# Kernel optimization log

Measured on AMD Instinct MI355X. Metric: run time of the kernel, lower is better.

The kernel has to match this reference:

```python
import jax, jax.numpy as jnp
import numpy as np

LR = 0.1  # inner-loop learning rate from `param - 0.1 * grad`

D = 4096          # memory width d; key/val are (1, d) per docstring
CTX = 512         # loss_context_size: number of keys per update step


def setup_inputs() -> dict:
    key = jax.random.key(0)
    k1, k2, k3 = jax.random.split(key, 3)
    W = jax.random.normal(k1, (D, D), dtype=jnp.float32) / np.sqrt(D)
    keys = jax.random.normal(k2, (CTX, D), dtype=jnp.float32)
    vals = jax.random.normal(k3, (CTX, D), dtype=jnp.float32)
    return {"W": W, "keys": keys, "vals": vals}


def reference(W, keys, vals):
    # OneStep.forward: preds_i = functional_forward(key_i, (W,)) = key_i @ W,
    # loss = MSE(preds, vals); new_W = W - 0.1 * dloss/dW.
    # The per-key loop is batched into a single (CTX, D) x (D, D) matmul.
    def loss_fn(Wp):
        preds = keys @ Wp  # (CTX, D)
        return jnp.mean((preds - vals) ** 2)

    g = jax.grad(loss_fn)(W)
    return W - LR * g
```

## Files before the change

kernel.cpp:

```cpp
#include <hip/hip_runtime.h>
#include <hip/hip_bf16.h>


typedef __bf16 bf16_t;
typedef __bf16 bf16x8 __attribute__((ext_vector_type(8)));
typedef float f32x4 __attribute__((ext_vector_type(4)));

#define D_DIM 4096
#define CTX_N 512
#define UPD_SCALE 9.5367431640625e-8f

__device__ __forceinline__ void gld16(const bf16_t* g, bf16_t* l) {
    __builtin_amdgcn_global_load_lds(
        (const __attribute__((address_space(1))) void*)g,
        (__attribute__((address_space(3))) void*)l, 16, 0, 0);
}

__device__ __forceinline__ void t_body2(
    float* tile, const float* __restrict__ src, bf16_t* __restrict__ dstT,
    bf16_t* __restrict__ dstN, int M, int N, int bx, int by)
{
    const int tid = threadIdx.x;
    const int C0 = bx * 64, R0 = by * 64;
    const int r  = tid >> 2, cs = (tid & 3) * 16;

    const float* s = src + (size_t)(R0 + r) * N + C0 + cs;
    float f[16];
#pragma unroll
    for (int u = 0; u < 4; ++u) {
        const float4 v = ((const float4*)s)[u];
        f[4 * u + 0] = v.x; f[4 * u + 1] = v.y; f[4 * u + 2] = v.z; f[4 * u + 3] = v.w;
    }
#pragma unroll
    for (int u = 0; u < 16; ++u) tile[r * 65 + cs + u] = f[u];

    if (dstN) {
        bf16x8 v0, v1;
#pragma unroll
        for (int u = 0; u < 8; ++u) { v0[u] = (bf16_t)f[u]; v1[u] = (bf16_t)f[8 + u]; }
        bf16_t* d = dstN + (size_t)(R0 + r) * N + C0 + cs;
        *(bf16x8*)d = v0; *(bf16x8*)(d + 8) = v1;
    }
    __syncthreads();

    bf16x8 o0, o1;
#pragma unroll
    for (int u = 0; u < 8; ++u) {
        o0[u] = (bf16_t)tile[(cs + u) * 65 + r];
        o1[u] = (bf16_t)tile[(cs + 8 + u) * 65 + r];
    }
    bf16_t* d = dstT + (size_t)(C0 + r) * M + R0 + cs;
    *(bf16x8*)d = o0; *(bf16x8*)(d + 8) = o1;
}

__global__ __launch_bounds__(256) void t_all(
    const float* __restrict__ W, const float* __restrict__ K,
    const float* __restrict__ V, bf16_t* __restrict__ Wt,
    bf16_t* __restrict__ Kt, bf16_t* __restrict__ Kb, bf16_t* __restrict__ Vt)
{
    __shared__ float tile[64 * 65];
    const int y = blockIdx.y;
    if (y < 64)      t_body2(tile, W, Wt, nullptr, D_DIM, D_DIM, blockIdx.x, y);
    else if (y < 72) t_body2(tile, K, Kt, Kb,      CTX_N, D_DIM, blockIdx.x, y - 64);
    else             t_body2(tile, V, Vt, nullptr, CTX_N, D_DIM, blockIdx.x, y - 72);
}



#define K1_COMPUTE(BSEL, WA, WB)                                             \
    {                                                                        \
        const bf16_t* As = (const bf16_t*)(reg + (BSEL) * 8192);             \
        const bf16_t* Bs = (const bf16_t*)(reg + 4096 + (BSEL) * 8192);      \
        __builtin_amdgcn_s_waitcnt(WA);                                      \
        bf16x8 af[4];                                                        \
        _Pragma("unroll")                                                    \
        for (int mi = 0; mi < 4; ++mi)                                       \
            af[mi] = *(const bf16x8*)(As + (mi * 16 + l15) * 32 + quad * 8); \
        __builtin_amdgcn_s_waitcnt(WB);                                      \
        bf16x8 bq[4];                                                        \
        _Pragma("unroll")                                                    \
        for (int ni = 0; ni < 4; ++ni)                                       \
            bq[ni] = *(const bf16x8*)(Bs + (ni * 16 + l15) * 32 + quad * 8); \
        _Pragma("unroll")                                                    \
        for (int mi = 0; mi < 4; ++mi)                                       \
            _Pragma("unroll")                                                \
            for (int ni = 0; ni < 4; ++ni)                                   \
                acc[mi][ni] = __builtin_amdgcn_mfma_f32_16x16x32_bf16(       \
                    af[mi], bq[ni], acc[mi][ni], 0, 0, 0);                   \
    }

__global__ __launch_bounds__(256) void k1_residual(
    const bf16_t* __restrict__ Wt, const bf16_t* __restrict__ Kb,
    const bf16_t* __restrict__ Vt, bf16_t* __restrict__ Rt)
{
    __shared__ __align__(16) char smem[65536];

    const int tid = threadIdx.x, wave = tid >> 6, lane = tid & 63;
    const int j0 = blockIdx.x * 64, c0 = blockIdx.y * 64;
    const int l15 = lane & 15, quad = lane >> 4;
    const int kw = wave * 1024;

    char* reg = smem + wave * 16384;

    f32x4 acc[4][4] = {};

    const int srow = lane >> 2, sseg = (lane & 3) * 8;
    const bf16_t* ga = Wt + (size_t)(j0 + srow) * D_DIM + kw + sseg;
    const bf16_t* gb = Kb + (size_t)(c0 + srow) * D_DIM + kw + sseg;

    auto stageA = [&](int bsel, int ko) {
        bf16_t* la = (bf16_t*)(reg + bsel * 8192) + lane * 8;
#pragma unroll
        for (int c = 0; c < 4; ++c)
            gld16(ga + ko + (size_t)(c * 16) * D_DIM, la + c * 512);
    };
    auto stageB = [&](int bsel, int ko) {
        bf16_t* lb = (bf16_t*)(reg + 4096 + bsel * 8192) + lane * 8;
#pragma unroll
        for (int c = 0; c < 4; ++c)
            gld16(gb + ko + (size_t)(c * 16) * D_DIM, lb + c * 512);
    };

    stageA(0, 0); stageB(0, 0);
#pragma unroll 1
    for (int t = 1; t <= 29; t += 2) {
        stageA(1, t * 32); stageB(1, t * 32);
        __builtin_amdgcn_sched_barrier(0);
        K1_COMPUTE(0, 0x0f7c, 0x0f78);
        stageA(0, (t + 1) * 32); stageB(0, (t + 1) * 32);
        __builtin_amdgcn_sched_barrier(0);
        K1_COMPUTE(1, 0x0f7c, 0x0f78);
    }
    stageA(1, 31 * 32); stageB(1, 31 * 32);
    __builtin_amdgcn_sched_barrier(0);
    K1_COMPUTE(0, 0x0f7c, 0x0f78);
    K1_COMPUTE(1, 0x0f74, 0x0f70);

    float* ep = (float*)smem;
    __syncthreads();
#pragma unroll
    for (int w = 0; w < 4; ++w) {
        if (wave == w) {
#pragma unroll
            for (int mi = 0; mi < 4; ++mi)
#pragma unroll
                for (int ni = 0; ni < 4; ++ni)
#pragma unroll
                    for (int r = 0; r < 4; ++r) {
                        const int row = mi * 16 + quad * 4 + r;
                        const int col = ni * 16 + l15;
                        if (w == 0) ep[row * 68 + col]  = acc[mi][ni][r];
                        else        ep[row * 68 + col] += acc[mi][ni][r];
                    }
        }
        __syncthreads();
    }

    {
        const int row = tid >> 2, cs = (tid & 3) * 16;
        const size_t rbase = (size_t)(j0 + row) * CTX_N + c0 + cs;
        float e[16];
#pragma unroll
        for (int u = 0; u < 4; ++u) {
            const float4 v = ((const float4*)(ep + row * 68 + cs))[u];
            e[4 * u + 0] = v.x; e[4 * u + 1] = v.y;
            e[4 * u + 2] = v.z; e[4 * u + 3] = v.w;
        }
        const bf16x8 v0 = *(const bf16x8*)(Vt + rbase);
        const bf16x8 v1 = *(const bf16x8*)(Vt + rbase + 8);
        bf16x8 o0, o1;
#pragma unroll
        for (int u = 0; u < 8; ++u) {
            o0[u] = (bf16_t)(e[u]     - (float)v0[u]);
            o1[u] = (bf16_t)(e[8 + u] - (float)v1[u]);
        }
        *(bf16x8*)(Rt + rbase)     = o0;
        *(bf16x8*)(Rt + rbase + 8) = o1;
    }
}


#define K2_COMPUTE(BSEL)                                                     \
    {                                                                        \
        const bf16_t* As = (const bf16_t*)(smem + (BSEL) * 16384);           \
        const bf16_t* Bs = (const bf16_t*)(smem + (BSEL) * 16384 + 8192);    \
        bf16x8 af[4], bq[4];                                                 \
        _Pragma("unroll")                                                    \
        for (int mi = 0; mi < 4; ++mi)                                       \
            af[mi] = *(const bf16x8*)(As + (wi + mi * 16 + l15) * 32 + quad * 8); \
        _Pragma("unroll")                                                    \
        for (int ni = 0; ni < 4; ++ni)                                       \
            bq[ni] = *(const bf16x8*)(Bs + (wj + ni * 16 + l15) * 32 + quad * 8); \
        _Pragma("unroll")                                                    \
        for (int mi = 0; mi < 4; ++mi)                                       \
            _Pragma("unroll")                                                \
            for (int ni = 0; ni < 4; ++ni)                                   \
                acc[mi][ni] = __builtin_amdgcn_mfma_f32_16x16x32_bf16(       \
                    af[mi], bq[ni], acc[mi][ni], 0, 0, 0);                   \
    }

__global__ __launch_bounds__(256) void k2_update(
    const bf16_t* __restrict__ Kt, const bf16_t* __restrict__ Rt,
    const float* __restrict__ W, float* __restrict__ out)
{
    __shared__ __align__(16) char smem[32768];

    const int tid = threadIdx.x;

    const int id = blockIdx.x + 32 * blockIdx.y;
    const int xp = (id >> 3) & 31;
    const int yp = (id & 7) + 8 * (id >> 8);
    const int j0 = xp * 128, i0 = yp * 128;

    const int lane = tid & 63, wave = tid >> 6;
    const int wi = (wave >> 1) * 64, wj = (wave & 1) * 64;
    const int l15 = lane & 15, quad = lane >> 4;

    f32x4 acc[4][4] = {};

    const bf16_t* ga = Kt + (size_t)(i0 + (tid >> 2)) * CTX_N + (tid & 3) * 8;
    const bf16_t* gb = Rt + (size_t)(j0 + (tid >> 2)) * CTX_N + (tid & 3) * 8;

    auto stage = [&](int bsel, int cc) {
        bf16_t* la = (bf16_t*)(smem + bsel * 16384) + tid * 8;
        bf16_t* lb = (bf16_t*)(smem + bsel * 16384 + 8192) + tid * 8;
        gld16(ga + cc, la);
        gld16(ga + cc + (size_t)64 * CTX_N, la + 64 * 32);
        gld16(gb + cc, lb);
        gld16(gb + cc + (size_t)64 * CTX_N, lb + 64 * 32);
    };

    stage(0, 0);
    __syncthreads();
#pragma unroll 1
    for (int t = 1; t <= 13; t += 2) {
        stage(1, t * 32);
        __builtin_amdgcn_sched_barrier(0);
        K2_COMPUTE(0);
        __syncthreads();
        stage(0, (t + 1) * 32);
        __builtin_amdgcn_sched_barrier(0);
        K2_COMPUTE(1);
        __syncthreads();
    }
    stage(1, 15 * 32);
    __builtin_amdgcn_sched_barrier(0);
    K2_COMPUTE(0);
    __syncthreads();
    K2_COMPUTE(1);

    const size_t base = (size_t)(i0 + wi + quad * 4) * D_DIM + j0 + wj + l15;
    const float* wp = W + base;
    float*       op = out + base;

    float w0[16], w1[16];
#pragma unroll
    for (int r = 0; r < 4; ++r)
#pragma unroll
        for (int ni = 0; ni < 4; ++ni)
            w0[r * 4 + ni] = wp[(size_t)r * D_DIM + ni * 16];

#pragma unroll
    for (int mi = 0; mi < 4; ++mi) {
        float* wcur = (mi & 1) ? w1 : w0;
        float* wnxt = (mi & 1) ? w0 : w1;
        if (mi < 3) {
#pragma unroll
            for (int r = 0; r < 4; ++r)
#pragma unroll
                for (int ni = 0; ni < 4; ++ni)
                    wnxt[r * 4 + ni] =
                        wp[(size_t)((mi + 1) * 16 + r) * D_DIM + ni * 16];
        }
#pragma unroll
        for (int r = 0; r < 4; ++r)
#pragma unroll
            for (int ni = 0; ni < 4; ++ni)
                op[(size_t)(mi * 16 + r) * D_DIM + ni * 16] =
                    wcur[r * 4 + ni] - UPD_SCALE * acc[mi][ni][r];
    }
}

extern "C" void kernel_launch(void* const* d_in, const int* in_sizes, int n_in,
                              void* d_out, int out_size, void* d_ws, size_t ws_size,
                              hipStream_t stream) {
    const float* W = (const float*)d_in[0];
    const float* K = (const float*)d_in[1];
    const float* V = (const float*)d_in[2];
    float* out = (float*)d_out;

    char* ws = (char*)d_ws;
    bf16_t* Wt = (bf16_t*)(ws);
    bf16_t* Kt = (bf16_t*)(ws + (size_t)32 * 1024 * 1024);
    bf16_t* Kb = (bf16_t*)(ws + (size_t)36 * 1024 * 1024);
    bf16_t* Vt = (bf16_t*)(ws + (size_t)40 * 1024 * 1024);
    bf16_t* Rt = (bf16_t*)(ws + (size_t)44 * 1024 * 1024);

    t_all      <<<dim3(64, 80), 256, 0, stream>>>(W, K, V, Wt, Kt, Kb, Vt);
    k1_residual<<<dim3(64, 8),  256, 0, stream>>>(Wt, Kb, Vt, Rt);
    k2_update  <<<dim3(32, 32), 256, 0, stream>>>(Kt, Rt, W, out);
}
```

Measured before the change: 199.7 us.

## Load k1 GEMM operands directly into registers with triple-buffered prefetch instead of LDS

The residual GEMM kernel k1 no longer stages W and K tiles through LDS with global_load_lds double buffering. Each lane now loads its MFMA fragments straight from global memory into registers, keeping three register buffers in flight so loads for later k-steps overlap with current MFMAs. The LDS allocation shrinks to just the epilogue reduction buffer, which removes LDS traffic and could raise occupancy. The costs are much higher VGPR use and uncoalesced 16-byte global loads spread across 16 rows per instruction.

```diff
diff --git a/kernel.cpp b/kernel.cpp
--- a/kernel.cpp
+++ b/kernel.cpp
@@ -67,76 +67,54 @@
 
 
 
-#define K1_COMPUTE(BSEL, WA, WB)                                             \
-    {                                                                        \
-        const bf16_t* As = (const bf16_t*)(reg + (BSEL) * 8192);             \
-        const bf16_t* Bs = (const bf16_t*)(reg + 4096 + (BSEL) * 8192);      \
-        __builtin_amdgcn_s_waitcnt(WA);                                      \
-        bf16x8 af[4];                                                        \
-        _Pragma("unroll")                                                    \
-        for (int mi = 0; mi < 4; ++mi)                                       \
-            af[mi] = *(const bf16x8*)(As + (mi * 16 + l15) * 32 + quad * 8); \
-        __builtin_amdgcn_s_waitcnt(WB);                                      \
-        bf16x8 bq[4];                                                        \
+#define K1_LOAD(AR, BR, T)                                                   \
+    _Pragma("unroll")                                                        \
+    for (int x = 0; x < 4; ++x) {                                            \
+        AR[x] = *(const bf16x8*)(pA + (size_t)(x * 16) * D_DIM + (T) * 32);  \
+        BR[x] = *(const bf16x8*)(pB + (size_t)(x * 16) * D_DIM + (T) * 32);  \
+    }
+
+#define K1_MFMA(AR, BR)                                                      \
+    _Pragma("unroll")                                                        \
+    for (int mi = 0; mi < 4; ++mi)                                           \
         _Pragma("unroll")                                                    \
         for (int ni = 0; ni < 4; ++ni)                                       \
-            bq[ni] = *(const bf16x8*)(Bs + (ni * 16 + l15) * 32 + quad * 8); \
-        _Pragma("unroll")                                                    \
-        for (int mi = 0; mi < 4; ++mi)                                       \
-            _Pragma("unroll")                                                \
-            for (int ni = 0; ni < 4; ++ni)                                   \
-                acc[mi][ni] = __builtin_amdgcn_mfma_f32_16x16x32_bf16(       \
-                    af[mi], bq[ni], acc[mi][ni], 0, 0, 0);                   \
-    }
+            acc[mi][ni] = __builtin_amdgcn_mfma_f32_16x16x32_bf16(           \
+                AR[mi], BR[ni], acc[mi][ni], 0, 0, 0);
 
 __global__ __launch_bounds__(256) void k1_residual(
     const bf16_t* __restrict__ Wt, const bf16_t* __restrict__ Kb,
     const bf16_t* __restrict__ Vt, bf16_t* __restrict__ Rt)
 {
-    __shared__ __align__(16) char smem[65536];
+    __shared__ __align__(16) float ep[64 * 68];
 
     const int tid = threadIdx.x, wave = tid >> 6, lane = tid & 63;
     const int j0 = blockIdx.x * 64, c0 = blockIdx.y * 64;
     const int l15 = lane & 15, quad = lane >> 4;
     const int kw = wave * 1024;
 
-    char* reg = smem + wave * 16384;
-
     f32x4 acc[4][4] = {};
 
-    const int srow = lane >> 2, sseg = (lane & 3) * 8;
-    const bf16_t* ga = Wt + (size_t)(j0 + srow) * D_DIM + kw + sseg;
-    const bf16_t* gb = Kb + (size_t)(c0 + srow) * D_DIM + kw + sseg;
-
-    auto stageA = [&](int bsel, int ko) {
-        bf16_t* la = (bf16_t*)(reg + bsel * 8192) + lane * 8;
-#pragma unroll
-        for (int c = 0; c < 4; ++c)
-            gld16(ga + ko + (size_t)(c * 16) * D_DIM, la + c * 512);
-    };
-    auto stageB = [&](int bsel, int ko) {
-        bf16_t* lb = (bf16_t*)(reg + 4096 + bsel * 8192) + lane * 8;
-#pragma unroll
-        for (int c = 0; c < 4; ++c)
-            gld16(gb + ko + (size_t)(c * 16) * D_DIM, lb + c * 512);
-    };
-
-    stageA(0, 0); stageB(0, 0);
+    const bf16_t* pA = Wt + (size_t)(j0 + l15) * D_DIM + kw + quad * 8;
+    const bf16_t* pB = Kb + (size_t)(c0 + l15) * D_DIM + kw + quad * 8;
+
+    bf16x8 a0[4], b0[4], a1[4], b1[4], a2[4], b2[4];
+
+    K1_LOAD(a0, b0, 0);
+    K1_LOAD(a1, b1, 1);
+    K1_LOAD(a2, b2, 2);
 #pragma unroll 1
-    for (int t = 1; t <= 29; t += 2) {
-        stageA(1, t * 32); stageB(1, t * 32);
-        __builtin_amdgcn_sched_barrier(0);
-        K1_COMPUTE(0, 0x0f7c, 0x0f78);
-        stageA(0, (t + 1) * 32); stageB(0, (t + 1) * 32);
-        __builtin_amdgcn_sched_barrier(0);
-        K1_COMPUTE(1, 0x0f7c, 0x0f78);
-    }
-    stageA(1, 31 * 32); stageB(1, 31 * 32);
-    __builtin_amdgcn_sched_barrier(0);
-    K1_COMPUTE(0, 0x0f7c, 0x0f78);
-    K1_COMPUTE(1, 0x0f74, 0x0f70);
-
-    float* ep = (float*)smem;
+    for (int t = 0; t < 27; t += 3) {
+        K1_MFMA(a0, b0); K1_LOAD(a0, b0, t + 3);
+        K1_MFMA(a1, b1); K1_LOAD(a1, b1, t + 4);
+        K1_MFMA(a2, b2); K1_LOAD(a2, b2, t + 5);
+    }
+    K1_MFMA(a0, b0); K1_LOAD(a0, b0, 30);
+    K1_MFMA(a1, b1); K1_LOAD(a1, b1, 31);
+    K1_MFMA(a2, b2);
+    K1_MFMA(a0, b0);
+    K1_MFMA(a1, b1);
+
     __syncthreads();
 #pragma unroll
     for (int w = 0; w < 4; ++w) {
```

New measurement: 225.6 us. 1.13x slower.
